# Performance work log

Measured on AMD Instinct MI355X. Metric: run time of the kernel, lower is better.

Reference implementation:

```python
import jax, jax.numpy as jnp
import numpy as np
from jax import lax

DIM = 128
HEADS = 4
HEAD_DIM = DIM // HEADS          # 32
SR = 2
BN_EPS = 1e-5


def setup_inputs() -> dict:
    key = jax.random.key(0)
    ks = jax.random.split(key, 16)
    B, N, C = 8, 3136, DIM
    H = W = 56
    Nkv = (H // SR) * (W // SR)  # 784
    s = 0.05
    inp = {
        "x": jax.random.normal(ks[0], (B, N, C), jnp.float32),
        "relative_pos": jax.random.normal(ks[1], (HEADS, N, Nkv), jnp.float32),
        "Wq": jax.random.normal(ks[2], (C, C), jnp.float32) * s,
        "bq": jnp.zeros((C,), jnp.float32),
        "Wk": jax.random.normal(ks[3], (C, C), jnp.float32) * s,
        "bk": jnp.zeros((C,), jnp.float32),
        "Wv": jax.random.normal(ks[4], (C, C), jnp.float32) * s,
        "bv": jnp.zeros((C,), jnp.float32),
        "conv_w": jax.random.normal(ks[5], (C, 1, SR, SR), jnp.float32) * s,  # depthwise OIHW
        "conv_b": jnp.zeros((C,), jnp.float32),
        "bn_gamma": jnp.ones((C,), jnp.float32),
        "bn_beta": jnp.zeros((C,), jnp.float32),
        "bn_mean": jax.random.normal(ks[6], (C,), jnp.float32) * 0.1,
        "bn_var": jax.random.uniform(ks[7], (C,), jnp.float32, 0.5, 1.5),
        "Wp": jax.random.normal(ks[8], (C, C), jnp.float32) * s,
        "bp": jnp.zeros((C,), jnp.float32),
        "H": H,
        "W": W,
    }
    return inp


def reference(x, relative_pos, Wq, bq, Wk, bk, Wv, bv, conv_w, conv_b,
              bn_gamma, bn_beta, bn_mean, bn_var, Wp, bp, H, W):
    B, N, C = x.shape
    scale = HEAD_DIM ** -0.5

    # q: (B, heads, N, head_dim)
    q = (x @ Wq + bq).reshape(B, N, HEADS, HEAD_DIM).transpose(0, 2, 1, 3)

    # spatial reduction: depthwise conv stride SR + BatchNorm (eval, running stats)
    x_img = x.transpose(0, 2, 1).reshape(B, C, H, W)
    y = lax.conv_general_dilated(
        x_img, conv_w, window_strides=(SR, SR), padding="VALID",
        feature_group_count=C,
        dimension_numbers=("NCHW", "OIHW", "NCHW")) + conv_b[None, :, None, None]
    inv = bn_gamma * lax.rsqrt(bn_var + BN_EPS)
    y = y * inv[None, :, None, None] + (bn_beta - bn_mean * inv)[None, :, None, None]
    x_ = y.reshape(B, C, -1).transpose(0, 2, 1)  # (B, Nkv, C)
    Nkv = x_.shape[1]

    k = (x_ @ Wk + bk).reshape(B, Nkv, HEADS, HEAD_DIM).transpose(0, 2, 1, 3)
    v = (x_ @ Wv + bv).reshape(B, Nkv, HEADS, HEAD_DIM).transpose(0, 2, 1, 3)

    attn = jnp.einsum("bhnd,bhmd->bhnm", q, k) * scale + relative_pos[None]
    attn = jax.nn.softmax(attn, axis=-1)
    out = jnp.einsum("bhnm,bhmd->bhnd", attn, v)
    out = out.transpose(0, 2, 1, 3).reshape(B, N, C)
    return out @ Wp + bp
```

## Files before the change

### kernel.cpp

```cpp
#include <hip/hip_runtime.h>
#include <hip/hip_bf16.h>

#define BATCH 8
#define NQ 3136
#define CDIM 128
#define NHEAD 4
#define HD 32
#define NKV 784
#define HIMG 56
#define SCALE 0.17677669529663687f

typedef __attribute__((ext_vector_type(8))) short bf8_t;
typedef __attribute__((ext_vector_type(4))) float f4_t;

using bf16 = __hip_bfloat16;
using u16  = unsigned short;

static __device__ __forceinline__ float b2f(bf16 v){ return __bfloat162float(v); }
static __device__ __forceinline__ bf16  f2b(float v){ return __float2bfloat16(v); }
static __device__ __forceinline__ short f2s(float v){
  union { bf16 b; short s; } u; u.b = f2b(v); return u.s;
}
static __device__ __forceinline__ float u16f(u16 x){
  union { u16 u; bf16 b; } c; c.u = x; return b2f(c.b);
}
static __device__ __forceinline__ float ld1(const void* p, size_t i, int f){
  return f ? b2f(((const bf16*)p)[i]) : ((const float*)p)[i];
}
static __device__ __forceinline__ float4 ld4f(const void* p, size_t i, int f){
  if (f){
    ushort4 u = *(const ushort4*)((const bf16*)p + i);
    return make_float4(u16f(u.x), u16f(u.y), u16f(u.z), u16f(u.w));
  }
  return *(const float4*)((const float*)p + i);
}
static __device__ __forceinline__ bf8_t ld8(const void* p, size_t i, int f){
  if (f) return *(const bf8_t*)((const bf16*)p + i);
  const float* fp = (const float*)p + i;
  float4 a = *(const float4*)fp;
  float4 b = *(const float4*)(fp + 4);
  bf8_t r;
  r[0]=f2s(a.x); r[1]=f2s(a.y); r[2]=f2s(a.z); r[3]=f2s(a.w);
  r[4]=f2s(b.x); r[5]=f2s(b.y); r[6]=f2s(b.z); r[7]=f2s(b.w);
  return r;
}
static __device__ __forceinline__ int detect_flag(const void* var_raw){
  const u16* h = (const u16*)var_raw;
  int lane = threadIdx.x & 63;
  bool ok = true;
  #pragma unroll
  for (int t = 0; t < 2; t++){
    union { u16 u; bf16 b; } cv; cv.u = h[lane + 64*t];
    float v = b2f(cv.b);
    ok = ok && (v > 0.3f) && (v < 1.7f);
  }
  return (__ballot(ok) == ~0ull) ? 1 : 0;
}

static __device__ __forceinline__ void mfma_row(
    const bf8_t a[4], const bf16* __restrict__ Wt, int m, int g, f4_t acc[8])
{
  #pragma unroll
  for (int ct = 0; ct < 8; ct++){
    f4_t c = {0.f,0.f,0.f,0.f};
    const bf16* bp = Wt + (size_t)(ct*16 + m)*CDIM + 8*g;
    #pragma unroll
    for (int ks = 0; ks < 4; ks++){
      bf8_t b = *(const bf8_t*)(bp + 32*ks);
      c = __builtin_amdgcn_mfma_f32_16x16x32_bf16(a[ks], b, c, 0,0,0);
    }
    acc[ct] = c;
  }
}

__global__ __launch_bounds__(256) void prep_kernel(
    const void* __restrict__ Wq, const void* __restrict__ Wk,
    const void* __restrict__ Wv, const void* __restrict__ Wp,
    const void* __restrict__ var, const void* __restrict__ cw,
    const void* __restrict__ cb, const void* __restrict__ gam,
    const void* __restrict__ bet, const void* __restrict__ mea,
    const void* __restrict__ bq, const void* __restrict__ bk,
    const void* __restrict__ bv, const void* __restrict__ bp,
    bf16* __restrict__ Wqt, bf16* __restrict__ Wkt,
    bf16* __restrict__ Wvt, bf16* __restrict__ Wpt,
    bf16* __restrict__ bqs, bf16* __restrict__ bks,
    bf16* __restrict__ bvs, bf16* __restrict__ bps,
    float* __restrict__ cwf, float* __restrict__ inv, float* __restrict__ shift2)
{
  int f = detect_flag(var);
  int idx = blockIdx.x*256 + threadIdx.x;
  int mat = idx >> 14;
  int e   = idx & 16383;
  int o = e >> 7, i = e & 127;
  const void* src; bf16* dst; float s = 1.f;
  if      (mat == 0){ src = Wq; dst = Wqt; s = SCALE; }
  else if (mat == 1){ src = Wk; dst = Wkt; }
  else if (mat == 2){ src = Wv; dst = Wvt; }
  else              { src = Wp; dst = Wpt; }
  dst[e] = f2b(ld1(src, (size_t)i*128 + o, f) * s);

  if (blockIdx.x == 0){
    int t = threadIdx.x;
    { int e2 = t;       cwf[(e2&3)*128 + (e2>>2)] = ld1(cw, e2, f); }
    { int e2 = t + 256; cwf[(e2&3)*128 + (e2>>2)] = ld1(cw, e2, f); }
    if (t < 128){
      bqs[t] = f2b(ld1(bq, t, f) * SCALE);
      bks[t] = f2b(ld1(bk, t, f));
      bvs[t] = f2b(ld1(bv, t, f));
      bps[t] = f2b(ld1(bp, t, f));
      float iv = ld1(gam, t, f) * rsqrtf(ld1(var, t, f) + 1e-5f);
      inv[t] = iv;
      shift2[t] = ld1(bet, t, f) - ld1(mea, t, f) * iv + ld1(cb, t, f) * iv;
    }
  }
}

__global__ __launch_bounds__(256) void fat_kernel(
    const void* __restrict__ x, const void* __restrict__ var,
    const float* __restrict__ cwf, const float* __restrict__ inv,
    const float* __restrict__ shift2, bf16* __restrict__ xr,
    const bf16* __restrict__ Wqt, const bf16* __restrict__ bqs,
    bf16* __restrict__ qbf,
    const void* __restrict__ rel, bf16* __restrict__ relb, int qblk)
{
  int f = detect_flag(var);
  if (blockIdx.x < 784){
    int idx = blockIdx.x*256 + threadIdx.x;
    int c0 = (idx & 31)*4;
    int t  = idx >> 5;
    int b  = t / NKV;
    int kv = t - b*NKV;
    int i = kv/28, j = kv - i*28;
    size_t base = (size_t)(b*NQ + 2*i*HIMG + 2*j)*CDIM + c0;
    float4 t0 = ld4f(x, base, f);
    float4 t1 = ld4f(x, base + CDIM, f);
    float4 t2 = ld4f(x, base + HIMG*CDIM, f);
    float4 t3 = ld4f(x, base + HIMG*CDIM + CDIM, f);
    float4 w0 = *(const float4*)(cwf + c0);
    float4 w1 = *(const float4*)(cwf + 128 + c0);
    float4 w2 = *(const float4*)(cwf + 256 + c0);
    float4 w3 = *(const float4*)(cwf + 384 + c0);
    float4 iv4 = *(const float4*)(inv + c0);
    float4 sh4 = *(const float4*)(shift2 + c0);
    union { u16 h[4]; uint2 u; } pk;
    float a;
    a = t0.x*w0.x + t1.x*w1.x + t2.x*w2.x + t3.x*w3.x; pk.h[0] = (u16)f2s(a*iv4.x + sh4.x);
    a = t0.y*w0.y + t1.y*w1.y + t2.y*w2.y + t3.y*w3.y; pk.h[1] = (u16)f2s(a*iv4.y + sh4.y);
    a = t0.z*w0.z + t1.z*w1.z + t2.z*w2.z + t3.z*w3.z; pk.h[2] = (u16)f2s(a*iv4.z + sh4.z);
    a = t0.w*w0.w + t1.w*w1.w + t2.w*w2.w + t3.w*w3.w; pk.h[3] = (u16)f2s(a*iv4.w + sh4.w);
    *(uint2*)(xr + (size_t)t*CDIM + c0) = pk.u;
  } else if ((int)blockIdx.x < 784 + qblk){
    int wave = threadIdx.x >> 6, lane = threadIdx.x & 63;
    int m = lane & 15, g = lane >> 4;
    int task = (blockIdx.x - 784)*4 + wave;
    int row0 = task*16;
    bf8_t a[4];
    #pragma unroll
    for (int ks = 0; ks < 4; ks++)
      a[ks] = ld8(x, (size_t)(row0 + m)*CDIM + 8*g + 32*ks, f);
    f4_t acc[8];
    mfma_row(a, Wqt, m, g, acc);
    #pragma unroll
    for (int ct = 0; ct < 8; ct++){
      int col = ct*16 + m;
      float bv = b2f(bqs[col]);
      #pragma unroll
      for (int r = 0; r < 4; r++)
        qbf[(size_t)(row0 + 4*g + r)*CDIM + col] = f2b(acc[ct][r] + bv);
    }
  } else {
    if (f) return;
    int bi = blockIdx.x - 784 - qblk;
    size_t gid = ((size_t)bi*256 + threadIdx.x)*8;
    const float* fp = (const float*)rel + gid;
    float4 a  = *(const float4*)fp;
    float4 b4 = *(const float4*)(fp + 4);
    union { u16 hh[8]; uint4 u4; } pk;
    pk.hh[0]=(u16)f2s(a.x);  pk.hh[1]=(u16)f2s(a.y);
    pk.hh[2]=(u16)f2s(a.z);  pk.hh[3]=(u16)f2s(a.w);
    pk.hh[4]=(u16)f2s(b4.x); pk.hh[5]=(u16)f2s(b4.y);
    pk.hh[6]=(u16)f2s(b4.z); pk.hh[7]=(u16)f2s(b4.w);
    *(uint4*)(relb + gid) = pk.u4;
  }
}

__global__ __launch_bounds__(256) void kv_kernel(
    const bf16* __restrict__ xr,
    const bf16* __restrict__ Wkt, const bf16* __restrict__ Wvt,
    const bf16* __restrict__ bks, const bf16* __restrict__ bvs,
    bf16* __restrict__ kbf, bf16* __restrict__ vtb)
{
  int wave = threadIdx.x >> 6, lane = threadIdx.x & 63;
  int m = lane & 15, g = lane >> 4;
  bool isK = blockIdx.x < 98;
  int bx = isK ? blockIdx.x : blockIdx.x - 98;
  int row0 = (bx*4 + wave)*16;
  bf8_t a[4];
  #pragma unroll
  for (int ks = 0; ks < 4; ks++)
    a[ks] = *(const bf8_t*)(xr + (size_t)(row0 + m)*CDIM + 8*g + 32*ks);
  f4_t acc[8];
  mfma_row(a, isK ? Wkt : Wvt, m, g, acc);

  if (isK){
    #pragma unroll
    for (int ct = 0; ct < 8; ct++){
      int col = ct*16 + m;
      float bv = b2f(bks[col]);
      #pragma unroll
      for (int r = 0; r < 4; r++)
        kbf[(size_t)(row0 + 4*g + r)*CDIM + col] = f2b(acc[ct][r] + bv);
    }
  } else {
    int b   = row0 / NKV;
    int kv0 = row0 - b*NKV + 4*g;
    #pragma unroll
    for (int ct = 0; ct < 8; ct++){
      int col = ct*16 + m;
      float bv = b2f(bvs[col]);
      int h = col >> 5, d = col & 31;
      union { bf16 hh[4]; uint2 u; } pk;
      #pragma unroll
      for (int r = 0; r < 4; r++) pk.hh[r] = f2b(acc[ct][r] + bv);
      *(uint2*)(vtb + (size_t)((b*NHEAD + h)*HD + d)*NKV + kv0) = pk.u;
    }
  }
}

template<int RM> struct RelV { using T = float4; };
template<> struct RelV<1> { using T = uint2; };

template<int RM>
static __device__ __forceinline__ typename RelV<RM>::T relld(const void* relp, int off){
  if constexpr (RM == 1) return *(const uint2*)((const bf16*)relp + off);
  else                   return *(const float4*)((const float*)relp + off);
}
template<int RM>
static __device__ __forceinline__ float relget(const typename RelV<RM>::T& v, int r){
  if constexpr (RM == 1){
    union { uint2 u; u16 h[4]; } c; c.u = v;
    return u16f(c.h[r]);
  } else {
    return r == 0 ? v.x : (r == 1 ? v.y : (r == 2 ? v.z : v.w));
  }
}
template<int RM>
static __device__ __forceinline__ void ldrel8(
    typename RelV<RM>::T rl[8], const void* relp, int off){
  #pragma unroll
  for (int t = 0; t < 8; t++) rl[t] = relld<RM>(relp, off + 16*t);
}

template<int RM, int PF>
static __device__ __forceinline__ void chunk128(
    int kv0,
    typename RelV<RM>::T rl[8], bf8_t kc[8],
    typename RelV<RM>::T rln[8], bf8_t kn[8],
    const void* __restrict__ relp, const bf16* __restrict__ kbase,
    const bf16* __restrict__ vb0, const bf16* __restrict__ vb1,
    bf16* __restrict__ pl, int m, int g, bf8_t q8,
    float& m_run, float& l_run, f4_t& O0, f4_t& O1)
{
  f4_t s[8];
  #pragma unroll
  for (int t = 0; t < 8; t++){
    f4_t z = {0.f,0.f,0.f,0.f};
    s[t] = __builtin_amdgcn_mfma_f32_16x16x32_bf16(kc[t], q8, z, 0,0,0);
  }
  if constexpr (PF == 2){
    #pragma unroll
    for (int t = 0; t < 8; t++)
      kn[t] = *(const bf8_t*)(kbase + (size_t)(kv0 + 128 + t*16)*CDIM);
  } else if constexpr (PF == 1){
    kn[0] = *(const bf8_t*)(kbase + (size_t)768*CDIM);
  }
  bf8_t v0[4], v1[4];
  #pragma unroll
  for (int ks = 0; ks < 4; ks++){
    v0[ks] = *(const bf8_t*)(vb0 + kv0 + ks*32 + 8*g);
    v1[ks] = *(const bf8_t*)(vb1 + kv0 + ks*32 + 8*g);
  }
  #pragma unroll
  for (int t = 0; t < 8; t++)
    #pragma unroll
    for (int r = 0; r < 4; r++)
      s[t][r] += relget<RM>(rl[t], r);
  if constexpr (PF == 2) ldrel8<RM>(rln, relp, kv0 + 128 + 4*g);
  else if constexpr (PF == 1) rln[0] = relld<RM>(relp, 768 + 4*g);
  float vmax = s[0][0];
  #pragma unroll
  for (int t = 0; t < 8; t++)
    #pragma unroll
    for (int r = 0; r < 4; r++)
      if (t + r > 0) vmax = fmaxf(vmax, s[t][r]);
  vmax = fmaxf(vmax, __shfl_xor(vmax, 16, 64));
  vmax = fmaxf(vmax, __shfl_xor(vmax, 32, 64));
  if (!__all(vmax <= m_run + 8.f)){
    float mn = fmaxf(m_run, vmax);
    float al = __expf(m_run - mn);
    m_run = mn;
    l_run *= al;
    float alT[4];
    #pragma unroll
    for (int r = 0; r < 4; r++) alT[r] = __shfl(al, 4*g + r, 64);
    #pragma unroll
    for (int r = 0; r < 4; r++){ O0[r] *= alT[r]; O1[r] *= alT[r]; }
  }
  float lsum = 0.f;
  #pragma unroll
  for (int t = 0; t < 8; t++){
    union { u16 h[4]; uint2 u; } pk;
    #pragma unroll
    for (int r = 0; r < 4; r++){
      float p = __expf(s[t][r] - m_run);
      lsum += p;
      pk.h[r] = (u16)f2s(p);
    }
    *(uint2*)(pl + m*136 + t*16 + 4*g) = pk.u;
  }
  l_run += lsum;
  #pragma unroll
  for (int ks = 0; ks < 4; ks++){
    bf8_t a8 = *(const bf8_t*)(pl + m*136 + ks*32 + 8*g);
    O0 = __builtin_amdgcn_mfma_f32_16x16x32_bf16(a8, v0[ks], O0, 0,0,0);
    O1 = __builtin_amdgcn_mfma_f32_16x16x32_bf16(a8, v1[ks], O1, 0,0,0);
  }
}

template<int RM>
static __device__ __forceinline__ void attn_run(
    const void* __restrict__ relp, const bf16* __restrict__ kbase,
    const bf16* __restrict__ vb0, const bf16* __restrict__ vb1,
    bf16* __restrict__ pl, int m, int g,
    bf8_t q8, float& m_run, float& l_run, f4_t& O0, f4_t& O1)
{
  using RT = typename RelV<RM>::T;
  RT rlA[8], rlB[8];
  bf8_t kA[8], kB[8];
  ldrel8<RM>(rlA, relp, 4*g);
  #pragma unroll
  for (int t = 0; t < 8; t++)
    kA[t] = *(const bf8_t*)(kbase + (size_t)(t*16)*CDIM);

  chunk128<RM,2>(0,   rlA,kA, rlB,kB, relp,kbase,vb0,vb1,pl,m,g,q8,m_run,l_run,O0,O1);
  chunk128<RM,2>(128, rlB,kB, rlA,kA, relp,kbase,vb0,vb1,pl,m,g,q8,m_run,l_run,O0,O1);
  chunk128<RM,2>(256, rlA,kA, rlB,kB, relp,kbase,vb0,vb1,pl,m,g,q8,m_run,l_run,O0,O1);
  chunk128<RM,2>(384, rlB,kB, rlA,kA, relp,kbase,vb0,vb1,pl,m,g,q8,m_run,l_run,O0,O1);
  chunk128<RM,2>(512, rlA,kA, rlB,kB, relp,kbase,vb0,vb1,pl,m,g,q8,m_run,l_run,O0,O1);
  chunk128<RM,1>(640, rlB,kB, rlA,kA, relp,kbase,vb0,vb1,pl,m,g,q8,m_run,l_run,O0,O1);

  {
    f4_t z = {0.f,0.f,0.f,0.f};
    f4_t s1 = __builtin_amdgcn_mfma_f32_16x16x32_bf16(kA[0], q8, z, 0,0,0);
    #pragma unroll
    for (int r = 0; r < 4; r++) s1[r] += relget<RM>(rlA[0], r);
    float vmax = fmaxf(fmaxf(s1[0], s1[1]), fmaxf(s1[2], s1[3]));
    vmax = fmaxf(vmax, __shfl_xor(vmax, 16, 64));
    vmax = fmaxf(vmax, __shfl_xor(vmax, 32, 64));
    if (!__all(vmax <= m_run + 8.f)){
      float mn = fmaxf(m_run, vmax);
      float al = __expf(m_run - mn);
      m_run = mn;
      l_run *= al;
      float alT[4];
      #pragma unroll
      for (int r = 0; r < 4; r++) alT[r] = __shfl(al, 4*g + r, 64);
      #pragma unroll
      for (int r = 0; r < 4; r++){ O0[r] *= alT[r]; O1[r] *= alT[r]; }
    }
    union { u16 h[4]; uint2 u; } pk;
    float lsum = 0.f;
    #pragma unroll
    for (int r = 0; r < 4; r++){
      float p = __expf(s1[r] - m_run);
      lsum += p;
      pk.h[r] = (u16)f2s(p);
    }
    *(uint2*)(pl + m*136 + 4*g) = pk.u;
    l_run += lsum;
    bf8_t a8, v0, v1;
    if (g >= 2){
      bf8_t z8 = {0,0,0,0,0,0,0,0};
      a8 = z8; v0 = z8; v1 = z8;
    } else {
      a8 = *(const bf8_t*)(pl + m*136 + 8*g);
      v0 = *(const bf8_t*)(vb0 + 768 + 8*g);
      v1 = *(const bf8_t*)(vb1 + 768 + 8*g);
    }
    O0 = __builtin_amdgcn_mfma_f32_16x16x32_bf16(a8, v0, O0, 0,0,0);
    O1 = __builtin_amdgcn_mfma_f32_16x16x32_bf16(a8, v1, O1, 0,0,0);
  }
}

template<int QF, int FB>
static __device__ __forceinline__ void attn_device(
    const bf16* __restrict__ qbf, const void* __restrict__ x,
    const bf16* __restrict__ Wqt, const bf16* __restrict__ bqs,
    const bf16* __restrict__ kb, const bf16* __restrict__ vtb,
    const void* __restrict__ rel, const bf16* __restrict__ relb,
    const void* __restrict__ var,
    void* __restrict__ dout, bf16* __restrict__ obf)
{
  int f = detect_flag(var);
  int lane = threadIdx.x & 63;
  int m = lane & 15, g = lane >> 4;
  int qt = blockIdx.x, h = blockIdx.y, b = blockIdx.z;
  int qrow0 = qt*16;

  __shared__ bf16 Plds[16*136];
  bf16* pl = Plds;

  bf8_t q8;
  if constexpr (QF == 0){
    q8 = *(const bf8_t*)(qbf + (size_t)(b*NQ + qrow0 + m)*CDIM + h*HD + 8*g);
  } else {
    bf8_t xa[4];
    #pragma unroll
    for (int ks = 0; ks < 4; ks++)
      xa[ks] = ld8(x, (size_t)(b*NQ + qrow0 + m)*CDIM + 8*g + 32*ks, f);
    f4_t qc0 = {0.f,0.f,0.f,0.f}, qc1 = {0.f,0.f,0.f,0.f};
    const bf16* wp0 = Wqt + (size_t)(h*HD + m)*CDIM + 8*g;
    const bf16* wp1 = Wqt + (size_t)(h*HD + 16 + m)*CDIM + 8*g;
    #pragma unroll
    for (int ks = 0; ks < 4; ks++){
      bf8_t w0 = *(const bf8_t*)(wp0 + 32*ks);
      bf8_t w1 = *(const bf8_t*)(wp1 + 32*ks);
      qc0 = __builtin_amdgcn_mfma_f32_16x16x32_bf16(xa[ks], w0, qc0, 0,0,0);
      qc1 = __builtin_amdgcn_mfma_f32_16x16x32_bf16(xa[ks], w1, qc1, 0,0,0);
    }
    float bv0 = b2f(bqs[h*HD + m]);
    float bv1 = b2f(bqs[h*HD + 16 + m]);
    #pragma unroll
    for (int r = 0; r < 4; r++){
      pl[(4*g + r)*136 + m]      = f2b(qc0[r] + bv0);
      pl[(4*g + r)*136 + 16 + m] = f2b(qc1[r] + bv1);
    }
    q8 = *(const bf8_t*)(pl + m*136 + 8*g);
  }

  const bf16* kbase = kb  + (size_t)(b*NKV + m)*CDIM + h*HD + 8*g;
  const bf16* vb0   = vtb + (size_t)((b*NHEAD + h)*HD + m)*NKV;
  const bf16* vb1   = vtb + (size_t)((b*NHEAD + h)*HD + 16 + m)*NKV;
  size_t rrow = ((size_t)h*NQ + qrow0 + m)*(size_t)NKV;

  float m_run = -1e30f, l_run = 0.f;
  f4_t O0 = {0.f,0.f,0.f,0.f}, O1 = {0.f,0.f,0.f,0.f};

  if constexpr (FB == 0){
    const void* rsrc = f ? (const void*)((const bf16*)rel + rrow)
                         : (const void*)(relb + rrow);
    attn_run<1>(rsrc, kbase, vb0, vb1, pl, m, g, q8, m_run, l_run, O0, O1);
  } else {
    if (f) attn_run<1>((const void*)((const bf16*)rel + rrow), kbase, vb0, vb1,
                       pl, m, g, q8, m_run, l_run, O0, O1);
    else   attn_run<0>((const void*)((const float*)rel + rrow), kbase, vb0, vb1,
                       pl, m, g, q8, m_run, l_run, O0, O1);
  }

  l_run += __shfl_xor(l_run, 16, 64);
  l_run += __shfl_xor(l_run, 32, 64);
  float lT[4];
  #pragma unroll
  for (int r = 0; r < 4; r++) lT[r] = __shfl(l_run, 4*g + r, 64);

  bf16* ob = f ? (bf16*)dout : obf;
  size_t orow = (size_t)(b*NQ + qrow0 + 4*g);
  #pragma unroll
  for (int r = 0; r < 4; r++){
    float iv = 1.0f / lT[r];
    ob[(orow + r)*CDIM + h*HD + m]      = f2b(O0[r] * iv);
    ob[(orow + r)*CDIM + h*HD + 16 + m] = f2b(O1[r] * iv);
  }
}

template<int QF>
__global__ __launch_bounds__(64) void attn_kernel(
    const bf16* __restrict__ qbf, const void* __restrict__ x,
    const bf16* __restrict__ Wqt, const bf16* __restrict__ bqs,
    const bf16* __restrict__ kb, const bf16* __restrict__ vtb,
    const void* __restrict__ rel, const bf16* __restrict__ relb,
    const void* __restrict__ var,
    void* __restrict__ dout, bf16* __restrict__ obf)
{
  attn_device<QF,0>(qbf, x, Wqt, bqs, kb, vtb, rel, relb, var, dout, obf);
}

__global__ __launch_bounds__(64) void attn_kernel_fb(
    const bf16* __restrict__ qbf, const void* __restrict__ x,
    const bf16* __restrict__ Wqt, const bf16* __restrict__ bqs,
    const bf16* __restrict__ kb, const bf16* __restrict__ vtb,
    const void* __restrict__ rel, const bf16* __restrict__ relb,
    const void* __restrict__ var,
    void* __restrict__ dout, bf16* __restrict__ obf)
{
  attn_device<1,1>(qbf, x, Wqt, bqs, kb, vtb, rel, relb, var, dout, obf);
}

__global__ __launch_bounds__(256) void proj_kernel(
    const bf16* A0, const bf16* A1, const bf16* __restrict__ Wt,
    const bf16* __restrict__ bias, void* outp, const void* __restrict__ var)
{
  int f = detect_flag(var);
  const bf16* A = f ? A0 : A1;
  int wave = threadIdx.x >> 6, lane = threadIdx.x & 63;
  int m = lane & 15, g = lane >> 4;
  int row0 = (blockIdx.x*4 + wave)*16;
  bf8_t a[4];
  #pragma unroll
  for (int ks = 0; ks < 4; ks++)
    a[ks] = *(const bf8_t*)(A + (size_t)(row0 + m)*CDIM + 8*g + 32*ks);
  f4_t acc[8];
  mfma_row(a, Wt, m, g, acc);
  #pragma unroll
  for (int ct = 0; ct < 8; ct++){
    int col = ct*16 + m;
    float bv = b2f(bias[col]);
    #pragma unroll
    for (int r = 0; r < 4; r++){
      size_t oi = (size_t)(row0 + 4*g + r)*CDIM + col;
      float v = acc[ct][r] + bv;
      if (f) ((bf16*)outp)[oi]  = f2b(v);
      else   ((float*)outp)[oi] = v;
    }
  }
}

extern "C" void kernel_launch(void* const* d_in, const int* in_sizes, int n_in,
                              void* d_out, int out_size, void* d_ws, size_t ws_size,
                              hipStream_t stream)
{
  const void* x   = d_in[0];
  const void* rel = d_in[1];
  const void* Wq  = d_in[2];
  const void* bq  = d_in[3];
  const void* Wk  = d_in[4];
  const void* bk  = d_in[5];
  const void* Wv  = d_in[6];
  const void* bv  = d_in[7];
  const void* cw  = d_in[8];
  const void* cb  = d_in[9];
  const void* gam = d_in[10];
  const void* bet = d_in[11];
  const void* mea = d_in[12];
  const void* var = d_in[13];
  const void* Wp  = d_in[14];
  const void* bp  = d_in[15];

  char* w = (char*)d_ws;
  auto alloc = [&](size_t bytes){
    char* p = w; w += (bytes + 255) & ~(size_t)255; return p;
  };
  bf16* Wqt = (bf16*)alloc(128*128*sizeof(bf16));
  bf16* Wkt = (bf16*)alloc(128*128*sizeof(bf16));
  bf16* Wvt = (bf16*)alloc(128*128*sizeof(bf16));
  bf16* Wpt = (bf16*)alloc(128*128*sizeof(bf16));
  bf16* bqs = (bf16*)alloc(128*sizeof(bf16));
  bf16* bks = (bf16*)alloc(128*sizeof(bf16));
  bf16* bvs = (bf16*)alloc(128*sizeof(bf16));
  bf16* bps = (bf16*)alloc(128*sizeof(bf16));
  float* cwf    = (float*)alloc(512*sizeof(float));
  float* inv    = (float*)alloc(128*sizeof(float));
  float* shift2 = (float*)alloc(128*sizeof(float));
  bf16* xr  = (bf16*)alloc((size_t)BATCH*NKV*CDIM*sizeof(bf16));
  bf16* kbf = (bf16*)alloc((size_t)BATCH*NKV*CDIM*sizeof(bf16));
  bf16* vtb = (bf16*)alloc((size_t)BATCH*NKV*CDIM*sizeof(bf16));
  bf16* obf = (bf16*)alloc((size_t)BATCH*NQ*CDIM*sizeof(bf16));

  size_t relb_bytes = (size_t)NHEAD*NQ*NKV*sizeof(bf16);
  bf16* relb = nullptr;
  if (((char*)d_ws + ws_size) - w >= (ptrdiff_t)(relb_bytes + 256))
    relb = (bf16*)alloc(relb_bytes);

  size_t qbf_bytes = (size_t)BATCH*NQ*CDIM*sizeof(bf16);
  bool use_q = relb &&
      ((((char*)d_ws + ws_size) - w) >= (ptrdiff_t)(qbf_bytes + 256));
  bf16* qbf = use_q ? (bf16*)alloc(qbf_bytes) : nullptr;

  int qblk = use_q ? 392 : 0;
  int rblk = relb  ? 4802 : 0;

  prep_kernel<<<256, 256, 0, stream>>>(Wq, Wk, Wv, Wp, var, cw, cb, gam, bet, mea,
                                       bq, bk, bv, bp,
                                       Wqt, Wkt, Wvt, Wpt, bqs, bks, bvs, bps,
                                       cwf, inv, shift2);
  fat_kernel<<<784 + qblk + rblk, 256, 0, stream>>>(
      x, var, cwf, inv, shift2, xr, Wqt, bqs, qbf, rel, relb, qblk);
  kv_kernel<<<196, 256, 0, stream>>>(xr, Wkt, Wvt, bks, bvs, kbf, vtb);
  dim3 ag(196, NHEAD, BATCH);
  if (relb){
    if (use_q)
      attn_kernel<0><<<ag, 64, 0, stream>>>(
          qbf, x, Wqt, bqs, kbf, vtb, rel, relb, var, d_out, obf);
    else
      attn_kernel<1><<<ag, 64, 0, stream>>>(
          qbf, x, Wqt, bqs, kbf, vtb, rel, relb, var, d_out, obf);
  } else {
    attn_kernel_fb<<<ag, 64, 0, stream>>>(
        qbf, x, Wqt, bqs, kbf, vtb, rel, relb, var, d_out, obf);
  }
  proj_kernel<<<392, 256, 0, stream>>>((const bf16*)d_out, obf, Wpt, bps, d_out, var);
}
```

Before: 223.3 us.

## Fuse conv into K/V projection and drop rel-pos bf16 precast pass

Merges the depthwise conv+BN reduction with the K/V projection kernel, staging the reduced tile in shared memory instead of writing and re-reading an xr buffer. Removes the separate pass that cast the fp32 relative_pos table to bf16 and the precomputed Q buffer; attention now reads fp32 rel directly and recomputes Q per block. This trades an extra pre-pass over the large rel table for wider fp32 reads inside attention, and uses only 98 blocks for the fused conv/KV kernel, which risks low occupancy.

```diff
diff --git a/kernel.cpp b/kernel.cpp
--- a/kernel.cpp
+++ b/kernel.cpp
@@ -115,19 +115,24 @@
   }
 }
 
-__global__ __launch_bounds__(256) void fat_kernel(
+__global__ __launch_bounds__(256) void kvconv_kernel(
     const void* __restrict__ x, const void* __restrict__ var,
     const float* __restrict__ cwf, const float* __restrict__ inv,
-    const float* __restrict__ shift2, bf16* __restrict__ xr,
-    const bf16* __restrict__ Wqt, const bf16* __restrict__ bqs,
-    bf16* __restrict__ qbf,
-    const void* __restrict__ rel, bf16* __restrict__ relb, int qblk)
+    const float* __restrict__ shift2,
+    const bf16* __restrict__ Wkt, const bf16* __restrict__ Wvt,
+    const bf16* __restrict__ bks, const bf16* __restrict__ bvs,
+    bf16* __restrict__ kbf, bf16* __restrict__ vtb)
 {
   int f = detect_flag(var);
-  if (blockIdx.x < 784){
-    int idx = blockIdx.x*256 + threadIdx.x;
-    int c0 = (idx & 31)*4;
-    int t  = idx >> 5;
+  __shared__ bf16 xl[64*136];
+  int row0 = blockIdx.x*64;
+
+  #pragma unroll
+  for (int it = 0; it < 8; it++){
+    int s  = it*256 + threadIdx.x;
+    int lr = s >> 5;
+    int c0 = (s & 31)*4;
+    int t  = row0 + lr;
     int b  = t / NKV;
     int kv = t - b*NKV;
     int i = kv/28, j = kv - i*28;
@@ -148,72 +153,36 @@
     a = t0.y*w0.y + t1.y*w1.y + t2.y*w2.y + t3.y*w3.y; pk.h[1] = (u16)f2s(a*iv4.y + sh4.y);
     a = t0.z*w0.z + t1.z*w1.z + t2.z*w2.z + t3.z*w3.z; pk.h[2] = (u16)f2s(a*iv4.z + sh4.z);
     a = t0.w*w0.w + t1.w*w1.w + t2.w*w2.w + t3.w*w3.w; pk.h[3] = (u16)f2s(a*iv4.w + sh4.w);
-    *(uint2*)(xr + (size_t)t*CDIM + c0) = pk.u;
-  } else if ((int)blockIdx.x < 784 + qblk){
-    int wave = threadIdx.x >> 6, lane = threadIdx.x & 63;
-    int m = lane & 15, g = lane >> 4;
-    int task = (blockIdx.x - 784)*4 + wave;
-    int row0 = task*16;
-    bf8_t a[4];
-    #pragma unroll
-    for (int ks = 0; ks < 4; ks++)
-      a[ks] = ld8(x, (size_t)(row0 + m)*CDIM + 8*g + 32*ks, f);
-    f4_t acc[8];
-    mfma_row(a, Wqt, m, g, acc);
-    #pragma unroll
-    for (int ct = 0; ct < 8; ct++){
-      int col = ct*16 + m;
-      float bv = b2f(bqs[col]);
-      #pragma unroll
-      for (int r = 0; r < 4; r++)
-        qbf[(size_t)(row0 + 4*g + r)*CDIM + col] = f2b(acc[ct][r] + bv);
-    }
-  } else {
-    if (f) return;
-    int bi = blockIdx.x - 784 - qblk;
-    size_t gid = ((size_t)bi*256 + threadIdx.x)*8;
-    const float* fp = (const float*)rel + gid;
-    float4 a  = *(const float4*)fp;
-    float4 b4 = *(const float4*)(fp + 4);
-    union { u16 hh[8]; uint4 u4; } pk;
-    pk.hh[0]=(u16)f2s(a.x);  pk.hh[1]=(u16)f2s(a.y);
-    pk.hh[2]=(u16)f2s(a.z);  pk.hh[3]=(u16)f2s(a.w);
-    pk.hh[4]=(u16)f2s(b4.x); pk.hh[5]=(u16)f2s(b4.y);
-    pk.hh[6]=(u16)f2s(b4.z); pk.hh[7]=(u16)f2s(b4.w);
-    *(uint4*)(relb + gid) = pk.u4;
-  }
-}
-
-__global__ __launch_bounds__(256) void kv_kernel(
-    const bf16* __restrict__ xr,
-    const bf16* __restrict__ Wkt, const bf16* __restrict__ Wvt,
-    const bf16* __restrict__ bks, const bf16* __restrict__ bvs,
-    bf16* __restrict__ kbf, bf16* __restrict__ vtb)
-{
+    *(uint2*)(xl + lr*136 + c0) = pk.u;
+  }
+  __syncthreads();
+
   int wave = threadIdx.x >> 6, lane = threadIdx.x & 63;
   int m = lane & 15, g = lane >> 4;
-  bool isK = blockIdx.x < 98;
-  int bx = isK ? blockIdx.x : blockIdx.x - 98;
-  int row0 = (bx*4 + wave)*16;
+  int r16 = wave*16;
   bf8_t a[4];
   #pragma unroll
   for (int ks = 0; ks < 4; ks++)
-    a[ks] = *(const bf8_t*)(xr + (size_t)(row0 + m)*CDIM + 8*g + 32*ks);
-  f4_t acc[8];
-  mfma_row(a, isK ? Wkt : Wvt, m, g, acc);
-
-  if (isK){
+    a[ks] = *(const bf8_t*)(xl + (r16 + m)*136 + 8*g + 32*ks);
+  int grow = row0 + r16;
+
+  {
+    f4_t acc[8];
+    mfma_row(a, Wkt, m, g, acc);
     #pragma unroll
     for (int ct = 0; ct < 8; ct++){
       int col = ct*16 + m;
       float bv = b2f(bks[col]);
       #pragma unroll
       for (int r = 0; r < 4; r++)
-        kbf[(size_t)(row0 + 4*g + r)*CDIM + col] = f2b(acc[ct][r] + bv);
-    }
-  } else {
-    int b   = row0 / NKV;
-    int kv0 = row0 - b*NKV + 4*g;
+        kbf[(size_t)(grow + 4*g + r)*CDIM + col] = f2b(acc[ct][r] + bv);
+    }
+  }
+  {
+    f4_t acc[8];
+    mfma_row(a, Wvt, m, g, acc);
+    int b2  = grow / NKV;
+    int kv0 = grow - b2*NKV + 4*g;
     #pragma unroll
     for (int ct = 0; ct < 8; ct++){
       int col = ct*16 + m;
@@ -222,7 +191,7 @@
       union { bf16 hh[4]; uint2 u; } pk;
       #pragma unroll
       for (int r = 0; r < 4; r++) pk.hh[r] = f2b(acc[ct][r] + bv);
-      *(uint2*)(vtb + (size_t)((b*NHEAD + h)*HD + d)*NKV + kv0) = pk.u;
+      *(uint2*)(vtb + (size_t)((b2*NHEAD + h)*HD + d)*NKV + kv0) = pk.u;
     }
   }
 }
@@ -392,13 +361,11 @@
   }
 }
 
-template<int QF, int FB>
-static __device__ __forceinline__ void attn_device(
-    const bf16* __restrict__ qbf, const void* __restrict__ x,
+__global__ __launch_bounds__(64) void attn_kernel(
+    const void* __restrict__ x,
     const bf16* __restrict__ Wqt, const bf16* __restrict__ bqs,
     const bf16* __restrict__ kb, const bf16* __restrict__ vtb,
-    const void* __restrict__ rel, const bf16* __restrict__ relb,
-    const void* __restrict__ var,
+    const void* __restrict__ rel, const void* __restrict__ var,
     void* __restrict__ dout, bf16* __restrict__ obf)
 {
   int f = detect_flag(var);
@@ -411,9 +378,7 @@
   bf16* pl = Plds;
 
   bf8_t q8;
-  if constexpr (QF == 0){
-    q8 = *(const bf8_t*)(qbf + (size_t)(b*NQ + qrow0 + m)*CDIM + h*HD + 8*g);
-  } else {
+  {
     bf8_t xa[4];
     #pragma unroll
     for (int ks = 0; ks < 4; ks++)
@@ -446,16 +411,10 @@
   float m_run = -1e30f, l_run = 0.f;
   f4_t O0 = {0.f,0.f,0.f,0.f}, O1 = {0.f,0.f,0.f,0.f};
 
-  if constexpr (FB == 0){
-    const void* rsrc = f ? (const void*)((const bf16*)rel + rrow)
-                         : (const void*)(relb + rrow);
-    attn_run<1>(rsrc, kbase, vb0, vb1, pl, m, g, q8, m_run, l_run, O0, O1);
-  } else {
-    if (f) attn_run<1>((const void*)((const bf16*)rel + rrow), kbase, vb0, vb1,
-                       pl, m, g, q8, m_run, l_run, O0, O1);
-    else   attn_run<0>((const void*)((const float*)rel + rrow), kbase, vb0, vb1,
-                       pl, m, g, q8, m_run, l_run, O0, O1);
-  }
+  if (f) attn_run<1>((const void*)((const bf16*)rel + rrow), kbase, vb0, vb1,
+                     pl, m, g, q8, m_run, l_run, O0, O1);
+  else   attn_run<0>((const void*)((const float*)rel + rrow), kbase, vb0, vb1,
+                     pl, m, g, q8, m_run, l_run, O0, O1);
 
   l_run += __shfl_xor(l_run, 16, 64);
   l_run += __shfl_xor(l_run, 32, 64);
@@ -471,29 +430,6 @@
     ob[(orow + r)*CDIM + h*HD + m]      = f2b(O0[r] * iv);
     ob[(orow + r)*CDIM + h*HD + 16 + m] = f2b(O1[r] * iv);
   }
-}
-
-template<int QF>
-__global__ __launch_bounds__(64) void attn_kernel(
-    const bf16* __restrict__ qbf, const void* __restrict__ x,
-    const bf16* __restrict__ Wqt, const bf16* __restrict__ bqs,
-    const bf16* __restrict__ kb, const bf16* __restrict__ vtb,
-    const void* __restrict__ rel, const bf16* __restrict__ relb,
-    const void* __restrict__ var,
-    void* __restrict__ dout, bf16* __restrict__ obf)
-{
-  attn_device<QF,0>(qbf, x, Wqt, bqs, kb, vtb, rel, relb, var, dout, obf);
-}
-
-__global__ __launch_bounds__(64) void attn_kernel_fb(
-    const bf16* __restrict__ qbf, const void* __restrict__ x,
-    const bf16* __restrict__ Wqt, const bf16* __restrict__ bqs,
-    const bf16* __restrict__ kb, const bf16* __restrict__ vtb,
-    const void* __restrict__ rel, const bf16* __restrict__ relb,
-    const void* __restrict__ var,
-    void* __restrict__ dout, bf16* __restrict__ obf)
-{
-  attn_device<1,1>(qbf, x, Wqt, bqs, kb, vtb, rel, relb, var, dout, obf);
 }
 
 __global__ __launch_bounds__(256) void proj_kernel(
@@ -561,42 +497,17 @@
   float* cwf    = (float*)alloc(512*sizeof(float));
   float* inv    = (float*)alloc(128*sizeof(float));
   float* shift2 = (float*)alloc(128*sizeof(float));
-  bf16* xr  = (bf16*)alloc((size_t)BATCH*NKV*CDIM*sizeof(bf16));
   bf16* kbf = (bf16*)alloc((size_t)BATCH*NKV*CDIM*sizeof(bf16));
   bf16* vtb = (bf16*)alloc((size_t)BATCH*NKV*CDIM*sizeof(bf16));
   bf16* obf = (bf16*)alloc((size_t)BATCH*NQ*CDIM*sizeof(bf16));
-
-  size_t relb_bytes = (size_t)NHEAD*NQ*NKV*sizeof(bf16);
-  bf16* relb = nullptr;
-  if (((char*)d_ws + ws_size) - w >= (ptrdiff_t)(relb_bytes + 256))
-    relb = (bf16*)alloc(relb_bytes);
-
-  size_t qbf_bytes = (size_t)BATCH*NQ*CDIM*sizeof(bf16);
-  bool use_q = relb &&
-      ((((char*)d_ws + ws_size) - w) >= (ptrdiff_t)(qbf_bytes + 256));
-  bf16* qbf = use_q ? (bf16*)alloc(qbf_bytes) : nullptr;
-
-  int qblk = use_q ? 392 : 0;
-  int rblk = relb  ? 4802 : 0;
 
   prep_kernel<<<256, 256, 0, stream>>>(Wq, Wk, Wv, Wp, var, cw, cb, gam, bet, mea,
                                        bq, bk, bv, bp,
                                        Wqt, Wkt, Wvt, Wpt, bqs, bks, bvs, bps,
                                        cwf, inv, shift2);
-  fat_kernel<<<784 + qblk + rblk, 256, 0, stream>>>(
-      x, var, cwf, inv, shift2, xr, Wqt, bqs, qbf, rel, relb, qblk);
-  kv_kernel<<<196, 256, 0, stream>>>(xr, Wkt, Wvt, bks, bvs, kbf, vtb);
+  kvconv_kernel<<<98, 256, 0, stream>>>(x, var, cwf, inv, shift2,
+                                        Wkt, Wvt, bks, bvs, kbf, vtb);
   dim3 ag(196, NHEAD, BATCH);
-  if (relb){
-    if (use_q)
-      attn_kernel<0><<<ag, 64, 0, stream>>>(
-          qbf, x, Wqt, bqs, kbf, vtb, rel, relb, var, d_out, obf);
-    else
-      attn_kernel<1><<<ag, 64, 0, stream>>>(
-          qbf, x, Wqt, bqs, kbf, vtb, rel, relb, var, d_out, obf);
-  } else {
-    attn_kernel_fb<<<ag, 64, 0, stream>>>(
-        qbf, x, Wqt, bqs, kbf, vtb, rel, relb, var, d_out, obf);
-  }
+  attn_kernel<<<ag, 64, 0, stream>>>(x, Wqt, bqs, kbf, vtb, rel, var, d_out, obf);
   proj_kernel<<<392, 256, 0, stream>>>((const bf16*)d_out, obf, Wpt, bps, d_out, var);
 }
```

Result: slower. 228.1 us (+2.2%).
